# Optimization experiments

Measured on AMD Instinct MI355X. Metric: run time of the kernel, lower is better.

## Reference

```python
import jax, jax.numpy as jnp
import numpy as np

N_NODES = 50000
N_EDGES = 800000
N_GRAPHS = 512
D = 128


def _gcn_layer(x, W, b, src, dst, norm):
    # PyG GCNConv: h = x @ W; out[i] = sum_{j->i} norm_ji * h[j]; out += b
    h = x @ W                                   # [N, D]
    msg = h[src] * norm[:, None]                # [E+N, D] gathered messages
    out = jax.ops.segment_sum(msg, dst, num_segments=N_NODES)
    return out + b


def setup_inputs() -> dict:
    key = jax.random.key(0)
    ks = jax.random.split(key, 9)
    inp = {
        "x": jax.random.normal(ks[0], (N_NODES, D), dtype=jnp.float32),
        "W1": jax.random.normal(ks[1], (D, D), dtype=jnp.float32) * 0.05,
        "b1": jax.random.normal(ks[2], (D,), dtype=jnp.float32) * 0.05,
        "W2": jax.random.normal(ks[3], (D, D), dtype=jnp.float32) * 0.05,
        "b2": jax.random.normal(ks[4], (D,), dtype=jnp.float32) * 0.05,
        "W3": jax.random.normal(ks[5], (D, D), dtype=jnp.float32) * 0.05,
        "b3": jax.random.normal(ks[6], (D,), dtype=jnp.float32) * 0.05,
        "edge_index": jax.random.randint(ks[7], (2, N_EDGES), 0, N_NODES, dtype=jnp.int64),
        "batch_vec": jnp.sort(jax.random.randint(ks[8], (N_NODES,), 0, N_GRAPHS, dtype=jnp.int64)),
    }
    return inp


def reference(x, W1, b1, W2, b2, W3, b3, edge_index, batch_vec):
    # Add self-loops (GCNConv default) and compute symmetric normalization.
    loops = jnp.arange(N_NODES, dtype=edge_index.dtype)
    src = jnp.concatenate([edge_index[0], loops])   # [E+N]
    dst = jnp.concatenate([edge_index[1], loops])   # [E+N]
    deg = jax.ops.segment_sum(jnp.ones_like(dst, dtype=x.dtype), dst,
                              num_segments=N_NODES)
    dis = jnp.where(deg > 0, jax.lax.rsqrt(jnp.maximum(deg, 1.0)), 0.0)
    norm = dis[src] * dis[dst]                      # [E+N]

    h = jax.nn.relu(_gcn_layer(x, W1, b1, src, dst, norm))
    h = jax.nn.relu(_gcn_layer(h, W2, b2, src, dst, norm))
    h = jax.nn.relu(_gcn_layer(h, W3, b3, src, dst, norm))

    # global_add_pool: per-graph sum over nodes.
    return jax.ops.segment_sum(h, batch_vec, num_segments=N_GRAPHS)  # [G, D]
```

## Files before the change

### kernel.cpp

```cpp
#include <hip/hip_runtime.h>

#define N_NODES 50000
#define N_EDGES 800000
#define N_GRAPHS 512
#define DIM 128
#define N_PAD 50048

#define BW_LOG 9
#define BWID 512
#define NB ((N_NODES + BWID - 1) / BWID)
#define CHUNK 4096
#define NCHUNK ((N_EDGES + CHUNK - 1) / CHUNK)

typedef unsigned int uint;
typedef unsigned short ushort;
typedef __attribute__((ext_vector_type(8))) short bf16x8;
typedef __attribute__((ext_vector_type(4))) float f32x4;

__device__ __forceinline__ ushort f2bf(float f) {
    uint u = __float_as_uint(f);
    return (ushort)((u + 0x7fffu + ((u >> 16) & 1u)) >> 16);
}
__device__ __forceinline__ float bf2f(ushort h) { return __uint_as_float((uint)h << 16); }
__device__ __forceinline__ float bflo(uint p) { return __uint_as_float(p << 16); }
__device__ __forceinline__ float bfhi(uint p) { return __uint_as_float(p & 0xffff0000u); }


__global__ __launch_bounds__(256) void bhist_k(const int* __restrict__ dst,
                                               int* __restrict__ bcnt_pad, int e) {
    __shared__ int h[NB];
    int t = threadIdx.x;
    for (int i = t; i < NB; i += 256) h[i] = 0;
    __syncthreads();
    int base = blockIdx.x * CHUNK;
    for (int i = t; i < CHUNK; i += 256) {
        int idx = base + i;
        if (idx < e) atomicAdd(&h[dst[idx] >> BW_LOG], 1);
    }
    __syncthreads();
    for (int i = t; i < NB; i += 256)
        if (h[i]) atomicAdd(&bcnt_pad[i << 4], h[i]);
}

__global__ void bscan_k(const int* __restrict__ bcnt_pad, int* __restrict__ bbase,
                        int* __restrict__ bcur_pad) {
    if (threadIdx.x == 0) {
        int run = 0;
        for (int b = 0; b < NB; b++) {
            bbase[b] = run;
            bcur_pad[b << 4] = run;
            run += bcnt_pad[b << 4];
        }
        bbase[NB] = run;
    }
}

__global__ __launch_bounds__(256) void bscat_k(const int* __restrict__ src,
                                               const int* __restrict__ dst,
                                               int* __restrict__ bcur_pad,
                                               uint* __restrict__ stage, int e) {
    __shared__ int h[NB];
    __shared__ int bb[NB];
    __shared__ int lc[NB];
    int t = threadIdx.x;
    for (int i = t; i < NB; i += 256) h[i] = 0;
    __syncthreads();
    int base = blockIdx.x * CHUNK;
    for (int i = t; i < CHUNK; i += 256) {
        int idx = base + i;
        if (idx < e) atomicAdd(&h[dst[idx] >> BW_LOG], 1);
    }
    __syncthreads();
    for (int i = t; i < NB; i += 256) {
        int c = h[i];
        bb[i] = c ? atomicAdd(&bcur_pad[i << 4], c) : 0;
        lc[i] = 0;
    }
    __syncthreads();
    for (int i = t; i < CHUNK; i += 256) {
        int idx = base + i;
        if (idx < e) {
            int d = dst[idx];
            int b = d >> BW_LOG;
            int r = atomicAdd(&lc[b], 1);
            stage[bb[b] + r] = ((uint)src[idx] << BW_LOG) | (uint)(d & (BWID - 1));
        }
    }
}

__global__ __launch_bounds__(256) void csr_k(const uint* __restrict__ stage,
                                             const int* __restrict__ bbase,
                                             int* __restrict__ row_ptr,
                                             float* __restrict__ dis,
                                             int* __restrict__ col) {
    __shared__ int hist[BWID];
    __shared__ int excl[BWID];
    __shared__ int ws[256];
    int b = blockIdx.x, t = threadIdx.x;
    int beg = bbase[b], end = bbase[b + 1];
    for (int i = t; i < BWID; i += 256) hist[i] = 0;
    __syncthreads();
    for (int i = beg + t; i < end; i += 256)
        atomicAdd(&hist[stage[i] & (BWID - 1)], 1);
    __syncthreads();
    int s = hist[2 * t] + hist[2 * t + 1];
    ws[t] = s;
    __syncthreads();
    for (int o = 1; o < 256; o <<= 1) {
        int v = ws[t];
        int add = (t >= o) ? ws[t - o] : 0;
        __syncthreads();
        ws[t] = v + add;
        __syncthreads();
    }
    int pre = (t == 0) ? 0 : ws[t - 1];
    excl[2 * t] = pre;
    excl[2 * t + 1] = pre + hist[2 * t];
    __syncthreads();
    int node0 = b * BWID;
    for (int i = t; i < BWID; i += 256) {
        int node = node0 + i;
        if (node < N_NODES) {
            row_ptr[node] = beg + excl[i];
            dis[node] = rsqrtf((float)(hist[i] + 1));
        } else if (node == N_NODES) {
            row_ptr[node] = beg + excl[i];
        }
    }
    __syncthreads();
    for (int i = t; i < BWID; i += 256) hist[i] = excl[i];
    __syncthreads();
    for (int i = beg + t; i < end; i += 256) {
        uint p = stage[i];
        int d9 = p & (BWID - 1);
        int r = atomicAdd(&hist[d9], 1);
        col[beg + r] = (int)(p >> BW_LOG);
    }
}


__global__ void wconv_k(const float* __restrict__ Wa, const float* __restrict__ Wb,
                        const float* __restrict__ Wc, ushort* __restrict__ Whi,
                        ushort* __restrict__ Wlo) {
    int i = blockIdx.x * 256 + threadIdx.x;
    int layer = i >> 14, r = i & 16383;
    const float* W = layer == 0 ? Wa : (layer == 1 ? Wb : Wc);
    int k = r >> 7, nn = r & 127;
    float w = W[r];
    ushort h = f2bf(w);
    size_t o = (size_t)layer * DIM * DIM + nn * 128 + k;
    Whi[o] = h;
    Wlo[o] = f2bf(w - bf2f(h));
}


template <typename TIn>
__global__ __launch_bounds__(256) void gemm_mfma_k(const TIn* __restrict__ X,
                                                   const ushort* __restrict__ Whi,
                                                   const ushort* __restrict__ Wlo,
                                                   ushort* __restrict__ H, int n) {
    __shared__ __align__(16) ushort lds[128 * 136];
    int t = threadIdx.x;

    auto stageW = [&](const ushort* Wsw) {
#pragma unroll
        for (int j = 0; j < 8; j++) {
            int idx8 = t + j * 256;
            int nn = idx8 >> 4;
            int k0 = (idx8 & 15) * 8;
            uint4 v = ((const uint4*)Wsw)[idx8];
            *(uint4*)&lds[nn * 136 + k0] = v;
        }
    };

    stageW(Whi);

    int w = t >> 6, l = t & 63;
    int quad = l >> 4, lr = l & 15;
    int arow = blockIdx.x * 64 + w * 16 + lr;
    int srow = arow < n ? arow : n - 1;

    bf16x8 a[4], alo[4];
#pragma unroll
    for (int q = 0; q < 4; q++) {
        if constexpr (sizeof(TIn) == 4) {
            const float4* xp = (const float4*)(X + (size_t)srow * DIM + q * 32 + quad * 8);
            float4 v0 = xp[0], v1 = xp[1];
            float f[8] = {v0.x, v0.y, v0.z, v0.w, v1.x, v1.y, v1.z, v1.w};
            bf16x8 ah, al;
#pragma unroll
            for (int j = 0; j < 8; j++) {
                ushort h = f2bf(f[j]);
                ah[j] = (short)h;
                al[j] = (short)f2bf(f[j] - bf2f(h));
            }
            a[q] = ah;
            alo[q] = al;
        } else {
            a[q] = *(const bf16x8*)(X + (size_t)srow * DIM + q * 32 + quad * 8);
        }
    }

    f32x4 acc[8];
#pragma unroll
    for (int c = 0; c < 8; c++) acc[c] = (f32x4){0.f, 0.f, 0.f, 0.f};

    __syncthreads();
#pragma unroll
    for (int q = 0; q < 4; q++) {
#pragma unroll
        for (int c = 0; c < 8; c++) {
            bf16x8 b = *(const bf16x8*)&lds[(c * 16 + lr) * 136 + q * 32 + quad * 8];
            acc[c] = __builtin_amdgcn_mfma_f32_16x16x32_bf16(a[q], b, acc[c], 0, 0, 0);
            if constexpr (sizeof(TIn) == 4)
                acc[c] = __builtin_amdgcn_mfma_f32_16x16x32_bf16(alo[q], b, acc[c], 0, 0, 0);
        }
    }

    __syncthreads();
    stageW(Wlo);
    __syncthreads();
#pragma unroll
    for (int q = 0; q < 4; q++) {
#pragma unroll
        for (int c = 0; c < 8; c++) {
            bf16x8 b = *(const bf16x8*)&lds[(c * 16 + lr) * 136 + q * 32 + quad * 8];
            acc[c] = __builtin_amdgcn_mfma_f32_16x16x32_bf16(a[q], b, acc[c], 0, 0, 0);
        }
    }

    __syncthreads();
#pragma unroll
    for (int c = 0; c < 8; c++) {
#pragma unroll
        for (int r = 0; r < 4; r++) {
            int rl = w * 16 + quad * 4 + r;
            lds[rl * 136 + c * 16 + lr] = f2bf(acc[c][r]);
        }
    }
    __syncthreads();
#pragma unroll
    for (int j = 0; j < 4; j++) {
        int idx = t + j * 256;
        int rl = idx >> 4, sl = idx & 15;
        int grow = blockIdx.x * 64 + rl;
        if (grow < n) {
            uint4 v = *(const uint4*)&lds[rl * 136 + sl * 8];
            ((uint4*)(H + (size_t)grow * DIM))[sl] = v;
        }
    }
}


__global__ __launch_bounds__(256) void agg_k(const ushort* __restrict__ H,
                                             const int* __restrict__ row_ptr,
                                             const int* __restrict__ col,
                                             const float* __restrict__ dis,
                                             const float* __restrict__ bias,
                                             ushort* __restrict__ Out, int n) {
    int node = blockIdx.x * 16 + (threadIdx.x >> 4);
    int lane = threadIdx.x & 15;
    if (node >= n) return;
    const ushort* Hl = H + lane * 8;
    float dn = dis[node];
    int beg = row_ptr[node], end = row_ptr[node + 1];

    uint4 pw = *(const uint4*)(Hl + (size_t)node * DIM);
    float a0 = dn * bflo(pw.x), a1 = dn * bfhi(pw.x);
    float a2 = dn * bflo(pw.y), a3 = dn * bfhi(pw.y);
    float a4 = dn * bflo(pw.z), a5 = dn * bfhi(pw.z);
    float a6 = dn * bflo(pw.w), a7 = dn * bfhi(pw.w);

    int e = beg;
    for (; e + 3 < end; e += 4) {
        int c0 = col[e], c1 = col[e + 1], c2 = col[e + 2], c3 = col[e + 3];
        float w0 = dis[c0], w1 = dis[c1], w2 = dis[c2], w3 = dis[c3];
        uint4 p0 = *(const uint4*)(Hl + (size_t)c0 * DIM);
        uint4 p1 = *(const uint4*)(Hl + (size_t)c1 * DIM);
        uint4 p2 = *(const uint4*)(Hl + (size_t)c2 * DIM);
        uint4 p3 = *(const uint4*)(Hl + (size_t)c3 * DIM);
        a0 += w0 * bflo(p0.x) + w1 * bflo(p1.x) + w2 * bflo(p2.x) + w3 * bflo(p3.x);
        a1 += w0 * bfhi(p0.x) + w1 * bfhi(p1.x) + w2 * bfhi(p2.x) + w3 * bfhi(p3.x);
        a2 += w0 * bflo(p0.y) + w1 * bflo(p1.y) + w2 * bflo(p2.y) + w3 * bflo(p3.y);
        a3 += w0 * bfhi(p0.y) + w1 * bfhi(p1.y) + w2 * bfhi(p2.y) + w3 * bfhi(p3.y);
        a4 += w0 * bflo(p0.z) + w1 * bflo(p1.z) + w2 * bflo(p2.z) + w3 * bflo(p3.z);
        a5 += w0 * bfhi(p0.z) + w1 * bfhi(p1.z) + w2 * bfhi(p2.z) + w3 * bfhi(p3.z);
        a6 += w0 * bflo(p0.w) + w1 * bflo(p1.w) + w2 * bflo(p2.w) + w3 * bflo(p3.w);
        a7 += w0 * bfhi(p0.w) + w1 * bfhi(p1.w) + w2 * bfhi(p2.w) + w3 * bfhi(p3.w);
    }
    for (; e < end; e++) {
        int c = col[e];
        float w = dis[c];
        uint4 p = *(const uint4*)(Hl + (size_t)c * DIM);
        a0 += w * bflo(p.x);
        a1 += w * bfhi(p.x);
        a2 += w * bflo(p.y);
        a3 += w * bfhi(p.y);
        a4 += w * bflo(p.z);
        a5 += w * bfhi(p.z);
        a6 += w * bflo(p.w);
        a7 += w * bfhi(p.w);
    }
    int d0 = lane * 8;
    a0 = fmaxf(a0 * dn + bias[d0], 0.f);
    a1 = fmaxf(a1 * dn + bias[d0 + 1], 0.f);
    a2 = fmaxf(a2 * dn + bias[d0 + 2], 0.f);
    a3 = fmaxf(a3 * dn + bias[d0 + 3], 0.f);
    a4 = fmaxf(a4 * dn + bias[d0 + 4], 0.f);
    a5 = fmaxf(a5 * dn + bias[d0 + 5], 0.f);
    a6 = fmaxf(a6 * dn + bias[d0 + 6], 0.f);
    a7 = fmaxf(a7 * dn + bias[d0 + 7], 0.f);
    uint4 o;
    o.x = (uint)f2bf(a0) | ((uint)f2bf(a1) << 16);
    o.y = (uint)f2bf(a2) | ((uint)f2bf(a3) << 16);
    o.z = (uint)f2bf(a4) | ((uint)f2bf(a5) << 16);
    o.w = (uint)f2bf(a6) | ((uint)f2bf(a7) << 16);
    *(uint4*)(Out + (size_t)node * DIM + d0) = o;
}


__global__ void pool_k(const ushort* __restrict__ H, const int* __restrict__ batch,
                       float* Out, int n) {
    int d = threadIdx.x;
    int n0 = blockIdx.x * 64;
    int gcur = -1;
    float s = 0.f;
    for (int i = 0; i < 64; i++) {
        int node = n0 + i;
        if (node >= n) break;
        int g = batch[node];
        if (g != gcur) {
            if (gcur >= 0) atomicAdd(&Out[gcur * DIM + d], s);
            gcur = g;
            s = 0.f;
        }
        s += bflo((uint)H[(size_t)node * DIM + d]);
    }
    if (gcur >= 0) atomicAdd(&Out[gcur * DIM + d], s);
}


extern "C" void kernel_launch(void* const* d_in, const int* in_sizes, int n_in,
                              void* d_out, int out_size, void* d_ws, size_t ws_size,
                              hipStream_t stream) {
    const float* x  = (const float*)d_in[0];
    const float* W1 = (const float*)d_in[1];
    const float* b1 = (const float*)d_in[2];
    const float* W2 = (const float*)d_in[3];
    const float* b2 = (const float*)d_in[4];
    const float* W3 = (const float*)d_in[5];
    const float* b3 = (const float*)d_in[6];
    const int*   ei = (const int*)d_in[7];
    const int*   bv = (const int*)d_in[8];
    float* out = (float*)d_out;

    const int N = N_NODES, E = N_EDGES;

    char* p = (char*)d_ws;
    auto alloc = [&](size_t bytes) -> void* {
        void* r = (void*)p;
        p += (bytes + 255) & ~(size_t)255;
        return r;
    };
    int*    bcnt_pad = (int*)alloc((size_t)NB * 16 * 4);
    int*    bcur_pad = (int*)alloc((size_t)NB * 16 * 4);
    int*    bbase    = (int*)alloc((size_t)(NB + 1) * 4);
    int*    row_ptr  = (int*)alloc((size_t)(N + 1) * 4);
    float*  dis      = (float*)alloc((size_t)N * 4);
    uint*   stage    = (uint*)alloc((size_t)E * 4);
    int*    col      = (int*)alloc((size_t)E * 4);
    ushort* B1       = (ushort*)alloc((size_t)N_PAD * DIM * 2);
    ushort* B2       = (ushort*)alloc((size_t)N_PAD * DIM * 2);

    ushort* Whi = (ushort*)stage;
    ushort* Wlo = Whi + (size_t)3 * DIM * DIM;

    const int* src = ei;
    const int* dst = ei + E;

    hipMemsetAsync(d_out, 0, (size_t)N_GRAPHS * DIM * sizeof(float), stream);
    hipMemsetAsync(bcnt_pad, 0, (size_t)NB * 16 * 4, stream);

    bhist_k<<<NCHUNK, 256, 0, stream>>>(dst, bcnt_pad, E);
    bscan_k<<<1, 64, 0, stream>>>(bcnt_pad, bbase, bcur_pad);
    bscat_k<<<NCHUNK, 256, 0, stream>>>(src, dst, bcur_pad, stage, E);
    csr_k<<<NB, 256, 0, stream>>>(stage, bbase, row_ptr, dis, col);

    wconv_k<<<192, 256, 0, stream>>>(W1, W2, W3, Whi, Wlo);

    int gemm_grid = N_PAD / 64;
    int agg_grid  = (N + 15) / 16;

    gemm_mfma_k<float><<<gemm_grid, 256, 0, stream>>>(x, Whi, Wlo, B1, N);
    agg_k<<<agg_grid, 256, 0, stream>>>(B1, row_ptr, col, dis, b1, B2, N);

    gemm_mfma_k<ushort><<<gemm_grid, 256, 0, stream>>>(B2, Whi + (size_t)DIM * DIM,
                                                       Wlo + (size_t)DIM * DIM, B1, N);
    agg_k<<<agg_grid, 256, 0, stream>>>(B1, row_ptr, col, dis, b2, B2, N);

    gemm_mfma_k<ushort><<<gemm_grid, 256, 0, stream>>>(B2, Whi + (size_t)2 * DIM * DIM,
                                                       Wlo + (size_t)2 * DIM * DIM, B1, N);
    agg_k<<<agg_grid, 256, 0, stream>>>(B1, row_ptr, col, dis, b3, B2, N);

    pool_k<<<(N + 63) / 64, 128, 0, stream>>>(B2, bv, out, N);
}
```

Before: 290.8 us.

## Fuse final aggregation with global pooling and parallelize bucket scan

New measurement: 288.0 us (median of 2 runs). Within noise of the previous version (-1.0%).

```diff
diff --git a/kernel.cpp b/kernel.cpp
--- a/kernel.cpp
+++ b/kernel.cpp
@@ -44,15 +44,24 @@
 
 __global__ void bscan_k(const int* __restrict__ bcnt_pad, int* __restrict__ bbase,
                         int* __restrict__ bcur_pad) {
-    if (threadIdx.x == 0) {
-        int run = 0;
-        for (int b = 0; b < NB; b++) {
-            bbase[b] = run;
-            bcur_pad[b << 4] = run;
-            run += bcnt_pad[b << 4];
-        }
-        bbase[NB] = run;
-    }
+    __shared__ int v[128];
+    int t = threadIdx.x;
+    int x = (t < NB) ? bcnt_pad[t << 4] : 0;
+    v[t] = x;
+    __syncthreads();
+    for (int o = 1; o < 128; o <<= 1) {
+        int val = v[t];
+        int add = (t >= o) ? v[t - o] : 0;
+        __syncthreads();
+        v[t] = val + add;
+        __syncthreads();
+    }
+    if (t < NB) {
+        int excl = (t == 0) ? 0 : v[t - 1];
+        bbase[t] = excl;
+        bcur_pad[t << 4] = excl;
+    }
+    if (t == NB - 1) bbase[NB] = v[t];
 }
 
 __global__ __launch_bounds__(256) void bscat_k(const int* __restrict__ src,
@@ -252,6 +261,50 @@
 }
 
 
+#define AGG_BODY                                                                 \
+    const ushort* Hl = H + lane * 8;                                             \
+    float dn = dis[node];                                                        \
+    int beg = row_ptr[node], end = row_ptr[node + 1];                            \
+    uint4 pw = *(const uint4*)(Hl + (size_t)node * DIM);                         \
+    a0 = dn * bflo(pw.x); a1 = dn * bfhi(pw.x);                                  \
+    a2 = dn * bflo(pw.y); a3 = dn * bfhi(pw.y);                                  \
+    a4 = dn * bflo(pw.z); a5 = dn * bfhi(pw.z);                                  \
+    a6 = dn * bflo(pw.w); a7 = dn * bfhi(pw.w);                                  \
+    int e = beg;                                                                 \
+    for (; e + 3 < end; e += 4) {                                                \
+        int c0 = col[e], c1 = col[e + 1], c2 = col[e + 2], c3 = col[e + 3];      \
+        float w0 = dis[c0], w1 = dis[c1], w2 = dis[c2], w3 = dis[c3];            \
+        uint4 p0 = *(const uint4*)(Hl + (size_t)c0 * DIM);                       \
+        uint4 p1 = *(const uint4*)(Hl + (size_t)c1 * DIM);                       \
+        uint4 p2 = *(const uint4*)(Hl + (size_t)c2 * DIM);                       \
+        uint4 p3 = *(const uint4*)(Hl + (size_t)c3 * DIM);                       \
+        a0 += w0 * bflo(p0.x) + w1 * bflo(p1.x) + w2 * bflo(p2.x) + w3 * bflo(p3.x); \
+        a1 += w0 * bfhi(p0.x) + w1 * bfhi(p1.x) + w2 * bfhi(p2.x) + w3 * bfhi(p3.x); \
+        a2 += w0 * bflo(p0.y) + w1 * bflo(p1.y) + w2 * bflo(p2.y) + w3 * bflo(p3.y); \
+        a3 += w0 * bfhi(p0.y) + w1 * bfhi(p1.y) + w2 * bfhi(p2.y) + w3 * bfhi(p3.y); \
+        a4 += w0 * bflo(p0.z) + w1 * bflo(p1.z) + w2 * bflo(p2.z) + w3 * bflo(p3.z); \
+        a5 += w0 * bfhi(p0.z) + w1 * bfhi(p1.z) + w2 * bfhi(p2.z) + w3 * bfhi(p3.z); \
+        a6 += w0 * bflo(p0.w) + w1 * bflo(p1.w) + w2 * bflo(p2.w) + w3 * bflo(p3.w); \
+        a7 += w0 * bfhi(p0.w) + w1 * bfhi(p1.w) + w2 * bfhi(p2.w) + w3 * bfhi(p3.w); \
+    }                                                                            \
+    for (; e < end; e++) {                                                       \
+        int c = col[e];                                                          \
+        float w = dis[c];                                                        \
+        uint4 p = *(const uint4*)(Hl + (size_t)c * DIM);                         \
+        a0 += w * bflo(p.x); a1 += w * bfhi(p.x);                                \
+        a2 += w * bflo(p.y); a3 += w * bfhi(p.y);                                \
+        a4 += w * bflo(p.z); a5 += w * bfhi(p.z);                                \
+        a6 += w * bflo(p.w); a7 += w * bfhi(p.w);                                \
+    }                                                                            \
+    a0 = fmaxf(a0 * dn + bias[d0], 0.f);                                         \
+    a1 = fmaxf(a1 * dn + bias[d0 + 1], 0.f);                                     \
+    a2 = fmaxf(a2 * dn + bias[d0 + 2], 0.f);                                     \
+    a3 = fmaxf(a3 * dn + bias[d0 + 3], 0.f);                                     \
+    a4 = fmaxf(a4 * dn + bias[d0 + 4], 0.f);                                     \
+    a5 = fmaxf(a5 * dn + bias[d0 + 5], 0.f);                                     \
+    a6 = fmaxf(a6 * dn + bias[d0 + 6], 0.f);                                     \
+    a7 = fmaxf(a7 * dn + bias[d0 + 7], 0.f);
+
 __global__ __launch_bounds__(256) void agg_k(const ushort* __restrict__ H,
                                              const int* __restrict__ row_ptr,
                                              const int* __restrict__ col,
@@ -261,55 +314,9 @@
     int node = blockIdx.x * 16 + (threadIdx.x >> 4);
     int lane = threadIdx.x & 15;
     if (node >= n) return;
-    const ushort* Hl = H + lane * 8;
-    float dn = dis[node];
-    int beg = row_ptr[node], end = row_ptr[node + 1];
-
-    uint4 pw = *(const uint4*)(Hl + (size_t)node * DIM);
-    float a0 = dn * bflo(pw.x), a1 = dn * bfhi(pw.x);
-    float a2 = dn * bflo(pw.y), a3 = dn * bfhi(pw.y);
-    float a4 = dn * bflo(pw.z), a5 = dn * bfhi(pw.z);
-    float a6 = dn * bflo(pw.w), a7 = dn * bfhi(pw.w);
-
-    int e = beg;
-    for (; e + 3 < end; e += 4) {
-        int c0 = col[e], c1 = col[e + 1], c2 = col[e + 2], c3 = col[e + 3];
-        float w0 = dis[c0], w1 = dis[c1], w2 = dis[c2], w3 = dis[c3];
-        uint4 p0 = *(const uint4*)(Hl + (size_t)c0 * DIM);
-        uint4 p1 = *(const uint4*)(Hl + (size_t)c1 * DIM);
-        uint4 p2 = *(const uint4*)(Hl + (size_t)c2 * DIM);
-        uint4 p3 = *(const uint4*)(Hl + (size_t)c3 * DIM);
-        a0 += w0 * bflo(p0.x) + w1 * bflo(p1.x) + w2 * bflo(p2.x) + w3 * bflo(p3.x);
-        a1 += w0 * bfhi(p0.x) + w1 * bfhi(p1.x) + w2 * bfhi(p2.x) + w3 * bfhi(p3.x);
-        a2 += w0 * bflo(p0.y) + w1 * bflo(p1.y) + w2 * bflo(p2.y) + w3 * bflo(p3.y);
-        a3 += w0 * bfhi(p0.y) + w1 * bfhi(p1.y) + w2 * bfhi(p2.y) + w3 * bfhi(p3.y);
-        a4 += w0 * bflo(p0.z) + w1 * bflo(p1.z) + w2 * bflo(p2.z) + w3 * bflo(p3.z);
-        a5 += w0 * bfhi(p0.z) + w1 * bfhi(p1.z) + w2 * bfhi(p2.z) + w3 * bfhi(p3.z);
-        a6 += w0 * bflo(p0.w) + w1 * bflo(p1.w) + w2 * bflo(p2.w) + w3 * bflo(p3.w);
-        a7 += w0 * bfhi(p0.w) + w1 * bfhi(p1.w) + w2 * bfhi(p2.w) + w3 * bfhi(p3.w);
-    }
-    for (; e < end; e++) {
-        int c = col[e];
-        float w = dis[c];
-        uint4 p = *(const uint4*)(Hl + (size_t)c * DIM);
-        a0 += w * bflo(p.x);
-        a1 += w * bfhi(p.x);
-        a2 += w * bflo(p.y);
-        a3 += w * bfhi(p.y);
-        a4 += w * bflo(p.z);
-        a5 += w * bfhi(p.z);
-        a6 += w * bflo(p.w);
-        a7 += w * bfhi(p.w);
-    }
     int d0 = lane * 8;
-    a0 = fmaxf(a0 * dn + bias[d0], 0.f);
-    a1 = fmaxf(a1 * dn + bias[d0 + 1], 0.f);
-    a2 = fmaxf(a2 * dn + bias[d0 + 2], 0.f);
-    a3 = fmaxf(a3 * dn + bias[d0 + 3], 0.f);
-    a4 = fmaxf(a4 * dn + bias[d0 + 4], 0.f);
-    a5 = fmaxf(a5 * dn + bias[d0 + 5], 0.f);
-    a6 = fmaxf(a6 * dn + bias[d0 + 6], 0.f);
-    a7 = fmaxf(a7 * dn + bias[d0 + 7], 0.f);
+    float a0, a1, a2, a3, a4, a5, a6, a7;
+    AGG_BODY
     uint4 o;
     o.x = (uint)f2bf(a0) | ((uint)f2bf(a1) << 16);
     o.y = (uint)f2bf(a2) | ((uint)f2bf(a3) << 16);
@@ -318,25 +325,44 @@
     *(uint4*)(Out + (size_t)node * DIM + d0) = o;
 }
 
-
-__global__ void pool_k(const ushort* __restrict__ H, const int* __restrict__ batch,
-                       float* Out, int n) {
-    int d = threadIdx.x;
-    int n0 = blockIdx.x * 64;
-    int gcur = -1;
-    float s = 0.f;
-    for (int i = 0; i < 64; i++) {
-        int node = n0 + i;
-        if (node >= n) break;
-        int g = batch[node];
-        if (g != gcur) {
-            if (gcur >= 0) atomicAdd(&Out[gcur * DIM + d], s);
-            gcur = g;
-            s = 0.f;
-        }
-        s += bflo((uint)H[(size_t)node * DIM + d]);
-    }
-    if (gcur >= 0) atomicAdd(&Out[gcur * DIM + d], s);
+__global__ __launch_bounds__(256) void agg_pool_k(const ushort* __restrict__ H,
+                                                  const int* __restrict__ row_ptr,
+                                                  const int* __restrict__ col,
+                                                  const float* __restrict__ dis,
+                                                  const float* __restrict__ bias,
+                                                  const int* __restrict__ batch,
+                                                  float* __restrict__ Out, int n) {
+    __shared__ float acc[DIM];
+    int t = threadIdx.x;
+    int node = blockIdx.x * 16 + (t >> 4);
+    int lane = t & 15;
+    int d0 = lane * 8;
+    float a0 = 0.f, a1 = 0.f, a2 = 0.f, a3 = 0.f, a4 = 0.f, a5 = 0.f, a6 = 0.f, a7 = 0.f;
+    int g = -1;
+    if (node < n) {
+        AGG_BODY
+        g = batch[node];
+    }
+    int first = blockIdx.x * 16;
+    int last = first + 15 < n ? first + 15 : n - 1;
+    int g0 = batch[first], g1 = batch[last];
+    for (int gr = g0; gr <= g1; gr++) {
+        if (t < DIM) acc[t] = 0.f;
+        __syncthreads();
+        if (g == gr) {
+            atomicAdd(&acc[d0], a0);
+            atomicAdd(&acc[d0 + 1], a1);
+            atomicAdd(&acc[d0 + 2], a2);
+            atomicAdd(&acc[d0 + 3], a3);
+            atomicAdd(&acc[d0 + 4], a4);
+            atomicAdd(&acc[d0 + 5], a5);
+            atomicAdd(&acc[d0 + 6], a6);
+            atomicAdd(&acc[d0 + 7], a7);
+        }
+        __syncthreads();
+        if (t < DIM) atomicAdd(&Out[gr * DIM + t], acc[t]);
+        __syncthreads();
+    }
 }
 
 
@@ -382,7 +408,7 @@
     hipMemsetAsync(bcnt_pad, 0, (size_t)NB * 16 * 4, stream);
 
     bhist_k<<<NCHUNK, 256, 0, stream>>>(dst, bcnt_pad, E);
-    bscan_k<<<1, 64, 0, stream>>>(bcnt_pad, bbase, bcur_pad);
+    bscan_k<<<1, 128, 0, stream>>>(bcnt_pad, bbase, bcur_pad);
     bscat_k<<<NCHUNK, 256, 0, stream>>>(src, dst, bcur_pad, stage, E);
     csr_k<<<NB, 256, 0, stream>>>(stage, bbase, row_ptr, dis, col);
 
@@ -400,7 +426,5 @@
 
     gemm_mfma_k<ushort><<<gemm_grid, 256, 0, stream>>>(B2, Whi + (size_t)2 * DIM * DIM,
                                                        Wlo + (size_t)2 * DIM * DIM, B1, N);
-    agg_k<<<agg_grid, 256, 0, stream>>>(B1, row_ptr, col, dis, b3, B2, N);
-
-    pool_k<<<(N + 63) / 64, 128, 0, stream>>>(B2, bv, out, N);
-}
+    agg_pool_k<<<agg_grid, 256, 0, stream>>>(B1, row_ptr, col, dis, b3, bv, out, N);
+}
```
